# Kernel optimization log

Measured on AMD Instinct MI355X. Metric: run time of the kernel, lower is better.

## Reference

```python
import jax, jax.numpy as jnp
import numpy as np

C = 32            # multiplicity per irrep (node irreps = 32x0e + 32x1o)
N_NODES = 50000
N_EDGES = 800000
R_DIM = 8         # radial embedding dim
R_HID = 8         # radial MLP hidden width
N_SPECIES = 5
AVG_NEIGH = 16.0
N_PATHS = 4       # 0ex0e->0e, 0ex1o->1o, 1ox0e->1o, 1ox1o->0e


def setup_inputs() -> dict:
    key = jax.random.key(0)
    ks = jax.random.split(key, 16)
    inp = {
        'node_features': jax.random.normal(ks[0], (N_NODES, 4 * C), jnp.float32),
        'edge_features': jax.random.normal(ks[1], (N_EDGES, 4), jnp.float32),
        'radial_embedding': jax.random.normal(ks[2], (N_EDGES, R_DIM), jnp.float32),
        'senders': jax.random.randint(ks[3], (N_EDGES,), 0, N_NODES),
        'receivers': jax.random.randint(ks[4], (N_EDGES,), 0, N_NODES),
        'node_species': jax.random.randint(ks[5], (N_NODES,), 0, N_SPECIES),
        # linear_up: per-irrep (block-diagonal) mixing
        'W_up_s': jax.random.normal(ks[6], (C, C), jnp.float32),
        'W_up_v': jax.random.normal(ks[7], (C, C), jnp.float32),
        # radial MLP (no biases, e3nn-style): R_DIM -> R_HID -> N_PATHS*C
        'W_r1': jax.random.normal(ks[8], (R_DIM, R_HID), jnp.float32),
        'W_r2': jax.random.normal(ks[9], (R_HID, N_PATHS * C), jnp.float32),
        # linear_down: 2C x 0e -> 2C (C feats + C gates); 2C x 1o -> C x 1o
        'W_down_s': jax.random.normal(ks[10], (2 * C, 2 * C), jnp.float32),
        'W_down_v': jax.random.normal(ks[11], (2 * C, C), jnp.float32),
        # species-indexed skip connection to gate irreps
        'W_skip_s': jax.random.normal(ks[12], (N_SPECIES, C, 2 * C), jnp.float32),
        'W_skip_v': jax.random.normal(ks[13], (N_SPECIES, C, C), jnp.float32),
    }
    return inp


def reference(node_features, edge_features, radial_embedding, senders, receivers,
              node_species, W_up_s, W_up_v, W_r1, W_r2, W_down_s, W_down_v,
              W_skip_s, W_skip_v):
    N = node_features.shape[0]
    inv_sqrt_C = 1.0 / np.sqrt(C)
    # split irreps: scalars [N,C] and vectors [N,C,3]
    s = node_features[:, :C]
    v = node_features[:, C:].reshape(N, C, 3)
    # ---- linear_up (block-diagonal irreps Linear, fan-in normalized) ----
    s_up = (s @ W_up_s) * inv_sqrt_C
    v_up = jnp.einsum('ncx,cd->ndx', v, W_up_v) * inv_sqrt_C
    # ---- radial MLP -> per-edge tensor-product path weights ----
    h = jax.nn.silu((radial_embedding @ W_r1) * (1.0 / np.sqrt(R_DIM)))
    w = ((h @ W_r2) * (1.0 / np.sqrt(R_HID))).reshape(-1, N_PATHS, C)  # [E,4,C]
    # ---- tensor product messages over edges ----
    sh0 = edge_features[:, 0]      # [E]  l=0
    sh1 = edge_features[:, 1:4]    # [E,3] l=1
    se = s_up[senders]             # [E,C]
    ve = v_up[senders]             # [E,C,3]
    m0 = jnp.concatenate([
        w[:, 0] * se * sh0[:, None],                                      # 0e x 0e -> 0e
        w[:, 3] * jnp.einsum('ecx,ex->ec', ve, sh1) * (1.0 / np.sqrt(3.0))  # 1o x 1o -> 0e
    ], axis=1)                                                            # [E,2C]
    m1 = jnp.concatenate([
        w[:, 1, :, None] * se[:, :, None] * sh1[:, None, :],              # 0e x 1o -> 1o
        w[:, 2, :, None] * ve * sh0[:, None, None],                       # 1o x 0e -> 1o
    ], axis=1)                                                            # [E,2C,3]
    # ---- scatter aggregate to receivers, normalize by sqrt(avg neigh) ----
    inv_sqrt_deg = 1.0 / np.sqrt(AVG_NEIGH)
    agg0 = jax.ops.segment_sum(m0, receivers, num_segments=N) * inv_sqrt_deg
    agg1 = jax.ops.segment_sum(m1, receivers, num_segments=N) * inv_sqrt_deg
    # ---- linear_down to gate irreps (2C x 0e: C feats + C gates; C x 1o) ----
    inv_sqrt_2C = 1.0 / np.sqrt(2 * C)
    sc = (agg0 @ W_down_s) * inv_sqrt_2C                     # [N,2C]
    vc = jnp.einsum('ncx,cd->ndx', agg1, W_down_v) * inv_sqrt_2C  # [N,C,3]
    # ---- species-indexed skip connection ----
    skip_s = jnp.einsum('nc,ncd->nd', s, W_skip_s[node_species]) * inv_sqrt_C
    skip_v = jnp.einsum('ncx,ncd->ndx', v, W_skip_v[node_species]) * inv_sqrt_C
    sc = 0.5 * (sc + skip_s)
    vc = 0.5 * (vc + skip_v)
    # ---- gated nonlinearity: silu on scalars, silu(gates) * vectors ----
    feats = jax.nn.silu(sc[:, :C])
    gates = jax.nn.silu(sc[:, C:])
    vg = vc * gates[:, :, None]
    return jnp.concatenate([feats, vg.reshape(N, 3 * C)], axis=1)  # [N,4C]
```

## Files before the change

kernel.cpp:

```cpp
#include <hip/hip_runtime.h>
#include <stdint.h>

__device__ __forceinline__ float b2f(unsigned short u) {
    union { uint32_t i; float f; } v; v.i = ((uint32_t)u) << 16; return v.f;
}
__device__ __forceinline__ unsigned short f2b(float f) {
    union { float f; uint32_t i; } v; v.f = f;
    uint32_t i = v.i;
    uint32_t r = (i + 0x7fffu + ((i >> 16) & 1u)) >> 16;
    return (unsigned short)r;
}
__device__ __forceinline__ float silu_f(float x) { return x / (1.f + __expf(-x)); }

template<bool BF>
__device__ __forceinline__ float ldin(const void* p, size_t i) {
    if (BF) return b2f(((const unsigned short*)p)[i]);
    return ((const float*)p)[i];
}
template<bool BF>
__device__ __forceinline__ void ld4(const void* p, size_t i, float o[4]) {
    if (BF) {
        const ushort4 u = *(const ushort4*)((const unsigned short*)p + i);
        o[0] = b2f(u.x); o[1] = b2f(u.y); o[2] = b2f(u.z); o[3] = b2f(u.w);
    } else {
        const float4 f = *(const float4*)((const float*)p + i);
        o[0] = f.x; o[1] = f.y; o[2] = f.z; o[3] = f.w;
    }
}
template<bool BF>
__device__ __forceinline__ void stout(void* p, size_t i, float v) {
    if (BF) ((unsigned short*)p)[i] = f2b(v);
    else    ((float*)p)[i] = v;
}

#define INV_SQRT_C   0.17677669529663687f
#define INV_SQRT_8   0.3535533905932738f
#define INV_SQRT_3   0.5773502691896258f
#define INV_SQRT_DEG 0.25f
#define INV_SQRT_2C  0.125f

__device__ __forceinline__ bool detect_bf(const void* nf) {
    const int lane = threadIdx.x & 63;
    const uint32_t w = ((const uint32_t*)nf)[lane];
    const uint32_t ex = (w >> 7) & 0xFFu;
    const unsigned long long m = __ballot(ex >= 96u && ex <= 130u);
    return __popcll(m) > 32;
}

template<bool BF>
__device__ __forceinline__ void prep_body(
    const void* __restrict__ nf, const void* __restrict__ Wus,
    const void* __restrict__ Wuv, const void* __restrict__ radial,
    const int* __restrict__ recv, const void* __restrict__ Wr1,
    unsigned short* __restrict__ stage, unsigned short* __restrict__ hbuf,
    int* __restrict__ counts, int* __restrict__ table,
    int* __restrict__ ovcnt, int* __restrict__ ovlist, int N, int E)
{
    const int tid = threadIdx.x;
    __shared__ float sin_[256];
    const int half = tid >> 7;
    const int t = tid & 127;
    const int npairs = (N + 1) >> 1;
    for (int pair = blockIdx.x; pair < npairs; pair += gridDim.x) {
        const int n = pair * 2 + half;
        __syncthreads();
        if (n < N) sin_[half * 128 + t] = ldin<BF>(nf, (size_t)n * 128 + t);
        __syncthreads();
        if (n < N) {
            const float* sb = &sin_[half * 128];
            float acc = 0.f;
            if (t < 32) {
                #pragma unroll 8
                for (int c = 0; c < 32; ++c) acc += sb[c] * ldin<BF>(Wus, c * 32 + t);
                stage[(size_t)n * 128 + t] = f2b(acc * INV_SQRT_C);
            } else {
                const int q = t - 32;
                const int x = q >> 5;
                const int d = q & 31;
                #pragma unroll 8
                for (int c = 0; c < 32; ++c) acc += sb[32 + c * 3 + x] * ldin<BF>(Wuv, c * 32 + d);
                stage[(size_t)n * 128 + 32 + x * 32 + d] = f2b(acc * INV_SQRT_C);
            }
        }
    }
    for (int base = blockIdx.x * 256; base < E; base += gridDim.x * 256) {
        const int e = base + tid;
        if (e >= E) continue;
        float r[8];
        ld4<BF>(radial, (size_t)e * 8, r);
        ld4<BF>(radial, (size_t)e * 8 + 4, r + 4);
        unsigned short h[8];
        #pragma unroll
        for (int j = 0; j < 8; ++j) {
            float pre = 0.f;
            #pragma unroll
            for (int k = 0; k < 8; ++k) pre += r[k] * ldin<BF>(Wr1, k * 8 + j);
            pre *= INV_SQRT_8;
            h[j] = f2b(silu_f(pre) * INV_SQRT_8);
        }
        ushort4* hp = (ushort4*)(hbuf + (size_t)e * 8);
        hp[0] = make_ushort4(h[0], h[1], h[2], h[3]);
        hp[1] = make_ushort4(h[4], h[5], h[6], h[7]);
        const int rr = recv[e];
        const int pos = atomicAdd(&counts[rr], 1);
        if (pos < 64) table[(size_t)rr * 64 + pos] = e;
        else          ovlist[atomicAdd(ovcnt, 1)] = e;
    }
}
__global__ __launch_bounds__(256) void k_prep(
    const void* nf, const void* Wus, const void* Wuv, const void* radial,
    const int* recv, const void* Wr1,
    unsigned short* stage, unsigned short* hbuf,
    int* counts, int* table, int* ovcnt, int* ovlist, int N, int E)
{
    if (detect_bf(nf)) prep_body<true >(nf, Wus, Wuv, radial, recv, Wr1, stage, hbuf,
                                        counts, table, ovcnt, ovlist, N, E);
    else               prep_body<false>(nf, Wus, Wuv, radial, recv, Wr1, stage, hbuf,
                                        counts, table, ovcnt, ovlist, N, E);
}

template<bool BF>
__device__ __forceinline__ void aggregate_body(
    const void* __restrict__ nf, const void* __restrict__ ef,
    const int* __restrict__ senders, const int* __restrict__ recv,
    const int* __restrict__ species,
    const void* __restrict__ Wr2, const void* __restrict__ Wds,
    const void* __restrict__ Wdv, const void* __restrict__ Wss,
    const void* __restrict__ Wsv,
    const unsigned short* __restrict__ stage,
    const unsigned short* __restrict__ hbuf,
    const int* __restrict__ counts, const int* __restrict__ table,
    const int* __restrict__ ovcnt, const int* __restrict__ ovlist,
    void* __restrict__ out, int N)
{
    __shared__ float lds_agg0[4][64];
    __shared__ float lds_agg1[4][3][65];
    __shared__ float lds_scf[4][64];
    const int wave = threadIdx.x >> 6;
    const int lane = threadIdx.x & 63;
    const int n = blockIdx.x * 4 + wave;
    const bool valid = (n < N);
    int sp = 0;

    if (valid) {
        sp = species[n];
        const int cnt = counts[n];

        const int colA = (lane < 32) ? lane : lane + 32;
        float wA[8], wB[8];
        #pragma unroll
        for (int j = 0; j < 8; ++j) {
            wA[j] = ldin<BF>(Wr2, j * 128 + colA);
            wB[j] = ldin<BF>(Wr2, j * 128 + colA + 32);
        }

        const int mc = (cnt < 64) ? cnt : 64;
        int snd_r = 0;
        uint32_t ef0 = 0, ef1 = 0, ef2 = 0, ef3 = 0;
        uint32_t h0 = 0, h1 = 0, h2 = 0, h3 = 0;
        if (lane < mc) {
            const int eid = table[(size_t)n * 64 + lane];
            snd_r = senders[eid];
            if (BF) {
                const uint2 t = *(const uint2*)((const unsigned short*)ef + (size_t)eid * 4);
                ef0 = t.x; ef1 = t.y;
            } else {
                const uint4 t = *(const uint4*)((const float*)ef + (size_t)eid * 4);
                ef0 = t.x; ef1 = t.y; ef2 = t.z; ef3 = t.w;
            }
            const uint4 th = *(const uint4*)(hbuf + (size_t)eid * 8);
            h0 = th.x; h1 = th.y; h2 = th.z; h3 = th.w;
        }

        float acc0 = 0.f, a1x = 0.f, a1y = 0.f, a1z = 0.f;
        const int d = lane - 32;

        unsigned short c0 = 0, c1 = 0, c2 = 0;
        if (mc > 0) {
            const int s0 = __shfl(snd_r, 0, 64);
            const unsigned short* rec = stage + (size_t)s0 * 128;
            if (lane < 32) { c0 = rec[lane]; }
            else { c0 = rec[32 + d]; c1 = rec[64 + d]; c2 = rec[96 + d]; }
        }
        #pragma unroll 2
        for (int i = 0; i < mc; ++i) {
            unsigned short n0 = 0, n1 = 0, n2 = 0;
            if (i + 1 < mc) {
                const int sn = __shfl(snd_r, i + 1, 64);
                const unsigned short* rec = stage + (size_t)sn * 128;
                if (lane < 32) { n0 = rec[lane]; }
                else { n0 = rec[32 + d]; n1 = rec[64 + d]; n2 = rec[96 + d]; }
            }
            float sh0, s1x, s1y, s1z;
            if (BF) {
                const uint32_t a = (uint32_t)__shfl((int)ef0, i, 64);
                const uint32_t b = (uint32_t)__shfl((int)ef1, i, 64);
                sh0 = b2f((unsigned short)(a & 0xFFFFu)); s1x = b2f((unsigned short)(a >> 16));
                s1y = b2f((unsigned short)(b & 0xFFFFu)); s1z = b2f((unsigned short)(b >> 16));
            } else {
                sh0 = __int_as_float(__shfl((int)ef0, i, 64));
                s1x = __int_as_float(__shfl((int)ef1, i, 64));
                s1y = __int_as_float(__shfl((int)ef2, i, 64));
                s1z = __int_as_float(__shfl((int)ef3, i, 64));
            }
            const uint32_t ua = (uint32_t)__shfl((int)h0, i, 64);
            const uint32_t ub = (uint32_t)__shfl((int)h1, i, 64);
            const uint32_t uc = (uint32_t)__shfl((int)h2, i, 64);
            const uint32_t ud = (uint32_t)__shfl((int)h3, i, 64);
            float h[8];
            h[0] = b2f((unsigned short)(ua & 0xFFFFu)); h[1] = b2f((unsigned short)(ua >> 16));
            h[2] = b2f((unsigned short)(ub & 0xFFFFu)); h[3] = b2f((unsigned short)(ub >> 16));
            h[4] = b2f((unsigned short)(uc & 0xFFFFu)); h[5] = b2f((unsigned short)(uc >> 16));
            h[6] = b2f((unsigned short)(ud & 0xFFFFu)); h[7] = b2f((unsigned short)(ud >> 16));
            const float vA = h[0] * wA[0] + h[1] * wA[1] + h[2] * wA[2] + h[3] * wA[3]
                           + h[4] * wA[4] + h[5] * wA[5] + h[6] * wA[6] + h[7] * wA[7];
            const float vB = h[0] * wB[0] + h[1] * wB[1] + h[2] * wB[2] + h[3] * wB[3]
                           + h[4] * wB[4] + h[5] * wB[5] + h[6] * wB[6] + h[7] * wB[7];
            if (lane < 32) {
                const float se = b2f(c0);
                acc0 += vA * se * sh0;
                const float tt = vB * se;
                a1x += tt * s1x; a1y += tt * s1y; a1z += tt * s1z;
            } else {
                const float vx = b2f(c0), vy = b2f(c1), vz = b2f(c2);
                acc0 += vB * (vx * s1x + vy * s1y + vz * s1z) * INV_SQRT_3;
                const float tt = vA * sh0;
                a1x += tt * vx; a1y += tt * vy; a1z += tt * vz;
            }
            c0 = n0; c1 = n1; c2 = n2;
        }
        if (cnt > 64) {
            const int oc = *ovcnt;
            for (int i2 = 0; i2 < oc; ++i2) {
                const int e = ovlist[i2];
                if (recv[e] != n) continue;
                const int s = senders[e];
                float efv[4];
                ld4<BF>(ef, (size_t)e * 4, efv);
                const float sh0 = efv[0], s1x = efv[1], s1y = efv[2], s1z = efv[3];
                float h[8];
                #pragma unroll
                for (int j = 0; j < 8; ++j) h[j] = b2f(hbuf[(size_t)e * 8 + j]);
                const float vA = h[0] * wA[0] + h[1] * wA[1] + h[2] * wA[2] + h[3] * wA[3]
                               + h[4] * wA[4] + h[5] * wA[5] + h[6] * wA[6] + h[7] * wA[7];
                const float vB = h[0] * wB[0] + h[1] * wB[1] + h[2] * wB[2] + h[3] * wB[3]
                               + h[4] * wB[4] + h[5] * wB[5] + h[6] * wB[6] + h[7] * wB[7];
                const unsigned short* rec = stage + (size_t)s * 128;
                if (lane < 32) {
                    const float se = b2f(rec[lane]);
                    acc0 += vA * se * sh0;
                    const float tt = vB * se;
                    a1x += tt * s1x; a1y += tt * s1y; a1z += tt * s1z;
                } else {
                    const float vx = b2f(rec[32 + d]), vy = b2f(rec[64 + d]), vz = b2f(rec[96 + d]);
                    acc0 += vB * (vx * s1x + vy * s1y + vz * s1z) * INV_SQRT_3;
                    const float tt = vA * sh0;
                    a1x += tt * vx; a1y += tt * vy; a1z += tt * vz;
                }
            }
        }
        lds_agg0[wave][lane]    = acc0 * INV_SQRT_DEG;
        lds_agg1[wave][0][lane] = a1x * INV_SQRT_DEG;
        lds_agg1[wave][1][lane] = a1y * INV_SQRT_DEG;
        lds_agg1[wave][2][lane] = a1z * INV_SQRT_DEG;
    }
    __syncthreads();
    if (valid) {
        float sc = 0.f;
        #pragma unroll 8
        for (int c = 0; c < 64; ++c) sc += lds_agg0[wave][c] * ldin<BF>(Wds, c * 64 + lane);
        sc *= INV_SQRT_2C;
        float ss = 0.f;
        #pragma unroll 8
        for (int c = 0; c < 32; ++c)
            ss += ldin<BF>(nf, (size_t)n * 128 + c) * ldin<BF>(Wss, (size_t)sp * 2048 + c * 64 + lane);
        ss *= INV_SQRT_C;
        lds_scf[wave][lane] = 0.5f * (sc + ss);
    }
    __syncthreads();
    if (valid) {
        #pragma unroll
        for (int rr = 0; rr < 2; ++rr) {
            const int p = lane + rr * 64;
            float outv;
            if (p < 32) {
                outv = silu_f(lds_scf[wave][p]);
            } else {
                const int o = p - 32;
                const int c = o / 3;
                const int x = o - 3 * c;
                float vc = 0.f;
                #pragma unroll 8
                for (int c2 = 0; c2 < 64; ++c2) vc += lds_agg1[wave][x][c2] * ldin<BF>(Wdv, c2 * 32 + c);
                vc *= INV_SQRT_2C;
                float sv = 0.f;
                #pragma unroll 8
                for (int c2 = 0; c2 < 32; ++c2)
                    sv += ldin<BF>(nf, (size_t)n * 128 + 32 + c2 * 3 + x) * ldin<BF>(Wsv, (size_t)sp * 1024 + c2 * 32 + c);
                sv *= INV_SQRT_C;
                const float g = silu_f(lds_scf[wave][32 + c]);
                outv = 0.5f * (vc + sv) * g;
            }
            stout<BF>(out, (size_t)n * 128 + p, outv);
        }
    }
}
__global__ __launch_bounds__(256) void k_aggregate(
    const void* nf, const void* ef, const int* senders, const int* recv,
    const int* species,
    const void* Wr2, const void* Wds, const void* Wdv, const void* Wss, const void* Wsv,
    const unsigned short* stage, const unsigned short* hbuf,
    const int* counts, const int* table, const int* ovcnt, const int* ovlist,
    void* out, int N)
{
    if (detect_bf(nf)) aggregate_body<true >(nf, ef, senders, recv, species,
                                             Wr2, Wds, Wdv, Wss, Wsv,
                                             stage, hbuf, counts, table, ovcnt, ovlist, out, N);
    else               aggregate_body<false>(nf, ef, senders, recv, species,
                                             Wr2, Wds, Wdv, Wss, Wsv,
                                             stage, hbuf, counts, table, ovcnt, ovlist, out, N);
}

extern "C" void kernel_launch(void* const* d_in, const int* in_sizes, int n_in,
                              void* d_out, int out_size, void* d_ws, size_t ws_size,
                              hipStream_t stream) {
    const void* nf      = d_in[0];
    const void* ef      = d_in[1];
    const void* radial  = d_in[2];
    const int*  senders = (const int*)d_in[3];
    const int*  recv    = (const int*)d_in[4];
    const int*  specie  = (const int*)d_in[5];
    const void* Wus = d_in[6];
    const void* Wuv = d_in[7];
    const void* Wr1 = d_in[8];
    const void* Wr2 = d_in[9];
    const void* Wds = d_in[10];
    const void* Wdv = d_in[11];
    const void* Wss = d_in[12];
    const void* Wsv = d_in[13];

    const int N = in_sizes[5];
    const int E = in_sizes[3];

    const size_t stageB = (size_t)N * 128 * 2;
    const size_t hbufB  = (size_t)E * 8 * 2;
    const size_t tableB = (size_t)N * 64 * 4;
    const size_t need   = stageB + hbufB + tableB + (size_t)(N + 1 + E) * 4;
    if (ws_size < need) return;

    char* ws = (char*)d_ws;
    unsigned short* stage = (unsigned short*)ws;
    unsigned short* hbuf  = (unsigned short*)(ws + stageB);
    int* table   = (int*)(ws + stageB + hbufB);
    int* counts  = (int*)(ws + stageB + hbufB + tableB);
    int* ovcnt   = counts + N;
    int* ovlist  = ovcnt + 1;

    hipMemsetAsync(counts, 0, (size_t)(N + 1) * sizeof(int), stream);

    k_prep<<<2048, 256, 0, stream>>>(nf, Wus, Wuv, radial, recv, Wr1,
                                     stage, hbuf, counts, table, ovcnt, ovlist, N, E);
    k_aggregate<<<(N + 3) / 4, 256, 0, stream>>>(nf, ef, senders, recv, specie,
                                                 Wr2, Wds, Wdv, Wss, Wsv,
                                                 stage, hbuf, counts, table, ovcnt, ovlist,
                                                 d_out, N);
}
```

Baseline: 444.5 us.

## Pad vector staging to 4-wide ushort4 and stage per-edge metadata in LDS

The staged up-projected node features are re-laid out to a 160-element record, with each vector channel stored as an interleaved x,y,z,pad ushort4. The gather then loads one vector per lane instead of three strided shorts, and the gather is prefetched two edges ahead. Per-edge attributes, radial hidden values and sender ids go into LDS once instead of being broadcast with many shuffles per edge. Node features are cached in LDS for the skip terms, and the prep kernel maps one wave per node. The cost is a staging buffer 25% larger and more LDS use per block.

```diff
diff --git a/kernel.cpp b/kernel.cpp
--- a/kernel.cpp
+++ b/kernel.cpp
@@ -56,36 +56,36 @@
     int* __restrict__ counts, int* __restrict__ table,
     int* __restrict__ ovcnt, int* __restrict__ ovlist, int N, int E)
 {
-    const int tid = threadIdx.x;
-    __shared__ float sin_[256];
-    const int half = tid >> 7;
-    const int t = tid & 127;
-    const int npairs = (N + 1) >> 1;
-    for (int pair = blockIdx.x; pair < npairs; pair += gridDim.x) {
-        const int n = pair * 2 + half;
-        __syncthreads();
-        if (n < N) sin_[half * 128 + t] = ldin<BF>(nf, (size_t)n * 128 + t);
-        __syncthreads();
-        if (n < N) {
-            const float* sb = &sin_[half * 128];
+    __shared__ float wsm[4][128];
+    const int wave = threadIdx.x >> 6;
+    const int lane = threadIdx.x & 63;
+    const int nwaves = gridDim.x * 4;
+    for (int n = blockIdx.x * 4 + wave; n < N; n += nwaves) {
+        wsm[wave][lane]      = ldin<BF>(nf, (size_t)n * 128 + lane);
+        wsm[wave][64 + lane] = ldin<BF>(nf, (size_t)n * 128 + 64 + lane);
+        if (lane < 32) {
             float acc = 0.f;
-            if (t < 32) {
-                #pragma unroll 8
-                for (int c = 0; c < 32; ++c) acc += sb[c] * ldin<BF>(Wus, c * 32 + t);
-                stage[(size_t)n * 128 + t] = f2b(acc * INV_SQRT_C);
-            } else {
-                const int q = t - 32;
-                const int x = q >> 5;
-                const int d = q & 31;
-                #pragma unroll 8
-                for (int c = 0; c < 32; ++c) acc += sb[32 + c * 3 + x] * ldin<BF>(Wuv, c * 32 + d);
-                stage[(size_t)n * 128 + 32 + x * 32 + d] = f2b(acc * INV_SQRT_C);
-            }
-        }
-    }
-    for (int base = blockIdx.x * 256; base < E; base += gridDim.x * 256) {
-        const int e = base + tid;
-        if (e >= E) continue;
+            #pragma unroll 8
+            for (int c = 0; c < 32; ++c) acc += wsm[wave][c] * ldin<BF>(Wus, c * 32 + lane);
+            stage[(size_t)n * 160 + lane] = f2b(acc * INV_SQRT_C);
+        } else {
+            const int dd = lane - 32;
+            float ax = 0.f, ay = 0.f, az = 0.f;
+            #pragma unroll 8
+            for (int c = 0; c < 32; ++c) {
+                const float wv = ldin<BF>(Wuv, c * 32 + dd);
+                ax += wsm[wave][32 + 3 * c    ] * wv;
+                ay += wsm[wave][32 + 3 * c + 1] * wv;
+                az += wsm[wave][32 + 3 * c + 2] * wv;
+            }
+            *(ushort4*)(stage + (size_t)n * 160 + 32 + 4 * dd) =
+                make_ushort4(f2b(ax * INV_SQRT_C), f2b(ay * INV_SQRT_C),
+                             f2b(az * INV_SQRT_C), (unsigned short)0);
+        }
+    }
+    for (int e = blockIdx.x * 256 + threadIdx.x; e < E; e += gridDim.x * 256) {
+        const int rr = recv[e];
+        const int pos = atomicAdd(&counts[rr], 1);
         float r[8];
         ld4<BF>(radial, (size_t)e * 8, r);
         ld4<BF>(radial, (size_t)e * 8 + 4, r + 4);
@@ -95,14 +95,11 @@
             float pre = 0.f;
             #pragma unroll
             for (int k = 0; k < 8; ++k) pre += r[k] * ldin<BF>(Wr1, k * 8 + j);
-            pre *= INV_SQRT_8;
-            h[j] = f2b(silu_f(pre) * INV_SQRT_8);
+            h[j] = f2b(silu_f(pre * INV_SQRT_8) * INV_SQRT_8);
         }
         ushort4* hp = (ushort4*)(hbuf + (size_t)e * 8);
         hp[0] = make_ushort4(h[0], h[1], h[2], h[3]);
         hp[1] = make_ushort4(h[4], h[5], h[6], h[7]);
-        const int rr = recv[e];
-        const int pos = atomicAdd(&counts[rr], 1);
         if (pos < 64) table[(size_t)rr * 64 + pos] = e;
         else          ovlist[atomicAdd(ovcnt, 1)] = e;
     }
@@ -133,139 +130,134 @@
     const int* __restrict__ ovcnt, const int* __restrict__ ovlist,
     void* __restrict__ out, int N)
 {
-    __shared__ float lds_agg0[4][64];
-    __shared__ float lds_agg1[4][3][65];
-    __shared__ float lds_scf[4][64];
+    __shared__ float ldsM[4][64][16];
+    __shared__ float ldsNF[4][128];
     const int wave = threadIdx.x >> 6;
     const int lane = threadIdx.x & 63;
     const int n = blockIdx.x * 4 + wave;
     const bool valid = (n < N);
-    int sp = 0;
+    const int d = lane - 32;
+    int sp = 0, cnt = 0, mc = 0;
+    float wA[8], wB[8];
+    float acc0 = 0.f, a1x = 0.f, a1y = 0.f, a1z = 0.f;
 
     if (valid) {
-        sp = species[n];
-        const int cnt = counts[n];
-
+        sp  = species[n];
+        cnt = counts[n];
+        mc  = (cnt < 64) ? cnt : 64;
         const int colA = (lane < 32) ? lane : lane + 32;
-        float wA[8], wB[8];
         #pragma unroll
         for (int j = 0; j < 8; ++j) {
             wA[j] = ldin<BF>(Wr2, j * 128 + colA);
             wB[j] = ldin<BF>(Wr2, j * 128 + colA + 32);
         }
-
-        const int mc = (cnt < 64) ? cnt : 64;
-        int snd_r = 0;
-        uint32_t ef0 = 0, ef1 = 0, ef2 = 0, ef3 = 0;
-        uint32_t h0 = 0, h1 = 0, h2 = 0, h3 = 0;
+        ldsNF[wave][lane]      = ldin<BF>(nf, (size_t)n * 128 + lane);
+        ldsNF[wave][64 + lane] = ldin<BF>(nf, (size_t)n * 128 + 64 + lane);
         if (lane < mc) {
             const int eid = table[(size_t)n * 64 + lane];
-            snd_r = senders[eid];
+            const int snd = senders[eid];
+            float e4[4];
             if (BF) {
-                const uint2 t = *(const uint2*)((const unsigned short*)ef + (size_t)eid * 4);
-                ef0 = t.x; ef1 = t.y;
+                const ushort4 u = *(const ushort4*)((const unsigned short*)ef + (size_t)eid * 4);
+                e4[0] = b2f(u.x); e4[1] = b2f(u.y); e4[2] = b2f(u.z); e4[3] = b2f(u.w);
             } else {
-                const uint4 t = *(const uint4*)((const float*)ef + (size_t)eid * 4);
-                ef0 = t.x; ef1 = t.y; ef2 = t.z; ef3 = t.w;
+                ld4<false>(ef, (size_t)eid * 4, e4);
             }
             const uint4 th = *(const uint4*)(hbuf + (size_t)eid * 8);
-            h0 = th.x; h1 = th.y; h2 = th.z; h3 = th.w;
-        }
-
-        float acc0 = 0.f, a1x = 0.f, a1y = 0.f, a1z = 0.f;
-        const int d = lane - 32;
-
-        unsigned short c0 = 0, c1 = 0, c2 = 0;
-        if (mc > 0) {
-            const int s0 = __shfl(snd_r, 0, 64);
-            const unsigned short* rec = stage + (size_t)s0 * 128;
-            if (lane < 32) { c0 = rec[lane]; }
-            else { c0 = rec[32 + d]; c1 = rec[64 + d]; c2 = rec[96 + d]; }
-        }
-        #pragma unroll 2
+            float* M = ldsM[wave][lane];
+            ((float4*)M)[0] = make_float4(e4[0], e4[1], e4[2], e4[3]);
+            ((float4*)M)[1] = make_float4(b2f((unsigned short)(th.x & 0xFFFFu)),
+                                          b2f((unsigned short)(th.x >> 16)),
+                                          b2f((unsigned short)(th.y & 0xFFFFu)),
+                                          b2f((unsigned short)(th.y >> 16)));
+            ((float4*)M)[2] = make_float4(b2f((unsigned short)(th.z & 0xFFFFu)),
+                                          b2f((unsigned short)(th.z >> 16)),
+                                          b2f((unsigned short)(th.w & 0xFFFFu)),
+                                          b2f((unsigned short)(th.w >> 16)));
+            M[12] = __int_as_float(snd);
+        }
+    }
+
+    if (valid && mc > 0) {
+        auto gather = [&](int idx) -> ushort4 {
+            const int snd = __float_as_int(ldsM[wave][idx][12]);
+            const unsigned short* rec = stage + (size_t)snd * 160;
+            if (lane < 32) return make_ushort4(rec[lane], (unsigned short)0,
+                                               (unsigned short)0, (unsigned short)0);
+            return *(const ushort4*)(rec + 32 + 4 * d);
+        };
+        ushort4 c0 = make_ushort4(0, 0, 0, 0), c1 = c0, c2 = c0;
+        c0 = gather(0);
+        if (mc > 1) c1 = gather(1);
         for (int i = 0; i < mc; ++i) {
-            unsigned short n0 = 0, n1 = 0, n2 = 0;
-            if (i + 1 < mc) {
-                const int sn = __shfl(snd_r, i + 1, 64);
-                const unsigned short* rec = stage + (size_t)sn * 128;
-                if (lane < 32) { n0 = rec[lane]; }
-                else { n0 = rec[32 + d]; n1 = rec[64 + d]; n2 = rec[96 + d]; }
-            }
-            float sh0, s1x, s1y, s1z;
-            if (BF) {
-                const uint32_t a = (uint32_t)__shfl((int)ef0, i, 64);
-                const uint32_t b = (uint32_t)__shfl((int)ef1, i, 64);
-                sh0 = b2f((unsigned short)(a & 0xFFFFu)); s1x = b2f((unsigned short)(a >> 16));
-                s1y = b2f((unsigned short)(b & 0xFFFFu)); s1z = b2f((unsigned short)(b >> 16));
+            if (i + 2 < mc) c2 = gather(i + 2);
+            const float4 e4 = ((const float4*)ldsM[wave][i])[0];
+            const float4 ha = ((const float4*)ldsM[wave][i])[1];
+            const float4 hb = ((const float4*)ldsM[wave][i])[2];
+            const float vA = ha.x * wA[0] + ha.y * wA[1] + ha.z * wA[2] + ha.w * wA[3]
+                           + hb.x * wA[4] + hb.y * wA[5] + hb.z * wA[6] + hb.w * wA[7];
+            const float vB = ha.x * wB[0] + ha.y * wB[1] + ha.z * wB[2] + ha.w * wB[3]
+                           + hb.x * wB[4] + hb.y * wB[5] + hb.z * wB[6] + hb.w * wB[7];
+            const float sh0 = e4.x, s1x = e4.y, s1y = e4.z, s1z = e4.w;
+            if (lane < 32) {
+                const float se = b2f(c0.x);
+                acc0 += vA * se * sh0;
+                const float tt = vB * se;
+                a1x += tt * s1x; a1y += tt * s1y; a1z += tt * s1z;
             } else {
-                sh0 = __int_as_float(__shfl((int)ef0, i, 64));
-                s1x = __int_as_float(__shfl((int)ef1, i, 64));
-                s1y = __int_as_float(__shfl((int)ef2, i, 64));
-                s1z = __int_as_float(__shfl((int)ef3, i, 64));
-            }
-            const uint32_t ua = (uint32_t)__shfl((int)h0, i, 64);
-            const uint32_t ub = (uint32_t)__shfl((int)h1, i, 64);
-            const uint32_t uc = (uint32_t)__shfl((int)h2, i, 64);
-            const uint32_t ud = (uint32_t)__shfl((int)h3, i, 64);
+                const float vx = b2f(c0.x), vy = b2f(c0.y), vz = b2f(c0.z);
+                acc0 += vB * (vx * s1x + vy * s1y + vz * s1z) * INV_SQRT_3;
+                const float tt = vA * sh0;
+                a1x += tt * vx; a1y += tt * vy; a1z += tt * vz;
+            }
+            c0 = c1; c1 = c2;
+        }
+    }
+    if (valid && cnt > 64) {
+        const int oc = *ovcnt;
+        for (int i2 = 0; i2 < oc; ++i2) {
+            const int e = ovlist[i2];
+            if (recv[e] != n) continue;
+            const int s = senders[e];
+            float efv[4];
+            ld4<BF>(ef, (size_t)e * 4, efv);
+            const float sh0 = efv[0], s1x = efv[1], s1y = efv[2], s1z = efv[3];
             float h[8];
-            h[0] = b2f((unsigned short)(ua & 0xFFFFu)); h[1] = b2f((unsigned short)(ua >> 16));
-            h[2] = b2f((unsigned short)(ub & 0xFFFFu)); h[3] = b2f((unsigned short)(ub >> 16));
-            h[4] = b2f((unsigned short)(uc & 0xFFFFu)); h[5] = b2f((unsigned short)(uc >> 16));
-            h[6] = b2f((unsigned short)(ud & 0xFFFFu)); h[7] = b2f((unsigned short)(ud >> 16));
+            #pragma unroll
+            for (int j = 0; j < 8; ++j) h[j] = b2f(hbuf[(size_t)e * 8 + j]);
             const float vA = h[0] * wA[0] + h[1] * wA[1] + h[2] * wA[2] + h[3] * wA[3]
                            + h[4] * wA[4] + h[5] * wA[5] + h[6] * wA[6] + h[7] * wA[7];
             const float vB = h[0] * wB[0] + h[1] * wB[1] + h[2] * wB[2] + h[3] * wB[3]
                            + h[4] * wB[4] + h[5] * wB[5] + h[6] * wB[6] + h[7] * wB[7];
+            const unsigned short* rec = stage + (size_t)s * 160;
             if (lane < 32) {
-                const float se = b2f(c0);
+                const float se = b2f(rec[lane]);
                 acc0 += vA * se * sh0;
                 const float tt = vB * se;
                 a1x += tt * s1x; a1y += tt * s1y; a1z += tt * s1z;
             } else {
-                const float vx = b2f(c0), vy = b2f(c1), vz = b2f(c2);
+                const ushort4 u = *(const ushort4*)(rec + 32 + 4 * d);
+                const float vx = b2f(u.x), vy = b2f(u.y), vz = b2f(u.z);
                 acc0 += vB * (vx * s1x + vy * s1y + vz * s1z) * INV_SQRT_3;
                 const float tt = vA * sh0;
                 a1x += tt * vx; a1y += tt * vy; a1z += tt * vz;
             }
-            c0 = n0; c1 = n1; c2 = n2;
-        }
-        if (cnt > 64) {
-            const int oc = *ovcnt;
-            for (int i2 = 0; i2 < oc; ++i2) {
-                const int e = ovlist[i2];
-                if (recv[e] != n) continue;
-                const int s = senders[e];
-                float efv[4];
-                ld4<BF>(ef, (size_t)e * 4, efv);
-                const float sh0 = efv[0], s1x = efv[1], s1y = efv[2], s1z = efv[3];
-                float h[8];
-                #pragma unroll
-                for (int j = 0; j < 8; ++j) h[j] = b2f(hbuf[(size_t)e * 8 + j]);
-                const float vA = h[0] * wA[0] + h[1] * wA[1] + h[2] * wA[2] + h[3] * wA[3]
-                               + h[4] * wA[4] + h[5] * wA[5] + h[6] * wA[6] + h[7] * wA[7];
-                const float vB = h[0] * wB[0] + h[1] * wB[1] + h[2] * wB[2] + h[3] * wB[3]
-                               + h[4] * wB[4] + h[5] * wB[5] + h[6] * wB[6] + h[7] * wB[7];
-                const unsigned short* rec = stage + (size_t)s * 128;
-                if (lane < 32) {
-                    const float se = b2f(rec[lane]);
-                    acc0 += vA * se * sh0;
-                    const float tt = vB * se;
-                    a1x += tt * s1x; a1y += tt * s1y; a1z += tt * s1z;
-                } else {
-                    const float vx = b2f(rec[32 + d]), vy = b2f(rec[64 + d]), vz = b2f(rec[96 + d]);
-                    acc0 += vB * (vx * s1x + vy * s1y + vz * s1z) * INV_SQRT_3;
-                    const float tt = vA * sh0;
-                    a1x += tt * vx; a1y += tt * vy; a1z += tt * vz;
-                }
-            }
-        }
+        }
+    }
+
+    __syncthreads();
+
+    float* base = &ldsM[0][0][0];
+    float (*lds_agg0)[64]    = (float(*)[64])   base;
+    float (*lds_agg1)[3][65] = (float(*)[3][65])(base + 256);
+    float (*lds_scf)[64]     = (float(*)[64])  (base + 1036);
+
+    if (valid) {
         lds_agg0[wave][lane]    = acc0 * INV_SQRT_DEG;
         lds_agg1[wave][0][lane] = a1x * INV_SQRT_DEG;
         lds_agg1[wave][1][lane] = a1y * INV_SQRT_DEG;
         lds_agg1[wave][2][lane] = a1z * INV_SQRT_DEG;
-    }
-    __syncthreads();
-    if (valid) {
+
         float sc = 0.f;
         #pragma unroll 8
         for (int c = 0; c < 64; ++c) sc += lds_agg0[wave][c] * ldin<BF>(Wds, c * 64 + lane);
@@ -273,12 +265,10 @@
         float ss = 0.f;
         #pragma unroll 8
         for (int c = 0; c < 32; ++c)
-            ss += ldin<BF>(nf, (size_t)n * 128 + c) * ldin<BF>(Wss, (size_t)sp * 2048 + c * 64 + lane);
+            ss += ldsNF[wave][c] * ldin<BF>(Wss, (size_t)sp * 2048 + c * 64 + lane);
         ss *= INV_SQRT_C;
         lds_scf[wave][lane] = 0.5f * (sc + ss);
-    }
-    __syncthreads();
-    if (valid) {
+
         #pragma unroll
         for (int rr = 0; rr < 2; ++rr) {
             const int p = lane + rr * 64;
@@ -291,12 +281,13 @@
                 const int x = o - 3 * c;
                 float vc = 0.f;
                 #pragma unroll 8
-                for (int c2 = 0; c2 < 64; ++c2) vc += lds_agg1[wave][x][c2] * ldin<BF>(Wdv, c2 * 32 + c);
+                for (int c2 = 0; c2 < 64; ++c2)
+                    vc += lds_agg1[wave][x][c2] * ldin<BF>(Wdv, c2 * 32 + c);
                 vc *= INV_SQRT_2C;
                 float sv = 0.f;
                 #pragma unroll 8
                 for (int c2 = 0; c2 < 32; ++c2)
-                    sv += ldin<BF>(nf, (size_t)n * 128 + 32 + c2 * 3 + x) * ldin<BF>(Wsv, (size_t)sp * 1024 + c2 * 32 + c);
+                    sv += ldsNF[wave][32 + c2 * 3 + x] * ldin<BF>(Wsv, (size_t)sp * 1024 + c2 * 32 + c);
                 sv *= INV_SQRT_C;
                 const float g = silu_f(lds_scf[wave][32 + c]);
                 outv = 0.5f * (vc + sv) * g;
@@ -342,7 +333,7 @@
     const int N = in_sizes[5];
     const int E = in_sizes[3];
 
-    const size_t stageB = (size_t)N * 128 * 2;
+    const size_t stageB = (size_t)N * 160 * 2;
     const size_t hbufB  = (size_t)E * 8 * 2;
     const size_t tableB = (size_t)N * 64 * 4;
     const size_t need   = stageB + hbufB + tableB + (size_t)(N + 1 + E) * 4;
```

Result: slower. 479.9 us (+8.0%).
